# Optimization experiments

Hardware: AMD Instinct MI355X
Metric: run time of the kernel (lower is better)

Reference implementation:

```python
import jax, jax.numpy as jnp
import numpy as np


def _build_tree(N: int, n: int, seed: int = 0):
    """Random forest encoded as parent pointers + sibling ranks.

    parents:  int32 [N+1]; parents[i] in [0, i) for i>0, root(0) and sentinel(N) -> N.
    child_pos: int32 [N+1]; rank among siblings (in_edges order); >= n means the
               one-hot code is all zeros (matches torch.eye rows beyond n, and roots).
    """
    rng = np.random.default_rng(seed)
    parents = np.empty(N + 1, dtype=np.int32)
    parents[0] = N                      # root -> sentinel
    parents[1:N] = rng.integers(0, np.arange(1, N))  # parent of i is an earlier node
    parents[N] = N                      # sentinel self-loop

    pa = parents[:N].astype(np.int64)
    order = np.argsort(pa, kind="stable")
    sorted_pa = pa[order]
    _, first_idx, inv = np.unique(sorted_pa, return_index=True, return_inverse=True)
    rank = np.arange(N) - first_idx[inv]           # sibling rank within each parent group
    child_pos = np.empty(N + 1, dtype=np.int32)
    child_pos[order] = rank.astype(np.int32)
    child_pos[0] = n                    # root has no parent -> zero code
    child_pos[N] = n                    # sentinel -> zero code
    return parents, child_pos


def setup_inputs() -> dict:
    N, n, k = 262144, 32, 16
    parents, child_pos = _build_tree(N, n)
    return {
        "parents": jnp.asarray(parents),
        "child_pos": jnp.asarray(child_pos),
        "n": n,
        "k": k,
    }


def reference(parents, child_pos, n, k):
    """pos_embeds[node] = concat_{t=0..k-1} onehot(child_pos(ancestor_t(node)), n).

    This is the closed form of the original layer-by-layer scatter:
      pos[child, :n]  = eye row (sibling rank one-hot)
      pos[child, n:]  = pos[parent, :-n]
    Roots keep all-zero codes (child_pos = n -> out-of-range one-hot = zeros).
    """
    N = parents.shape[0] - 1

    def step(cur, _):
        code = jax.nn.one_hot(child_pos[cur], n, dtype=jnp.float32)  # [N, n]
        return parents[cur], code

    _, codes = jax.lax.scan(step, jnp.arange(N, dtype=parents.dtype), None, length=k)
    # codes: [k, N, n] -> [N, k*n] with slot 0 (own code) first
    return jnp.transpose(codes, (1, 0, 2)).reshape(N, k * n)
```

## Files before the change

kernel.cpp:

```cpp
#include <hip/hip_runtime.h>


#define NN 32
#define KK 16

typedef float f32x4 __attribute__((ext_vector_type(4)));

__global__ __launch_bounds__(256) void pe_fused_stride(
    const int* __restrict__ parents,
    const int* __restrict__ child_pos,
    f32x4* __restrict__ out4, int N, int n_waves)
{
    const int lane = (int)(threadIdx.x & 63);
    const int wid  = (int)((blockIdx.x * blockDim.x + threadIdx.x) >> 6);

    unsigned int c[4];
    {
        int cur = lane * n_waves + wid;
        if (cur >= N) cur = N;
        #pragma unroll
        for (int w = 0; w < 4; ++w) {
            unsigned int u = 0;
            #pragma unroll
            for (int b = 0; b < 4; ++b) {
                const int cp = child_pos[cur];
                const unsigned int byte = (cp < NN) ? (unsigned int)cp : 0xFFu;
                u |= byte << (8 * b);
                cur = parents[cur];
            }
            c[w] = u;
        }
    }

    const bool hi32 = (lane >= 32);
    const int  sh   = ((lane >> 3) & 3) * 8;
    const int  q4   = (lane & 7) * 4;

    f32x4* wout = out4 + (size_t)wid * 128 + lane;
    const size_t step = (size_t)n_waves * 128;

    #pragma unroll 4
    for (int j = 0; j < 64; ++j) {
        const unsigned s0 = (unsigned)__builtin_amdgcn_readlane((int)c[0], j);
        const unsigned s1 = (unsigned)__builtin_amdgcn_readlane((int)c[1], j);
        const unsigned s2 = (unsigned)__builtin_amdgcn_readlane((int)c[2], j);
        const unsigned s3 = (unsigned)__builtin_amdgcn_readlane((int)c[3], j);

        const int code0 = (int)(((hi32 ? s1 : s0) >> sh) & 0xFFu);
        const int code1 = (int)(((hi32 ? s3 : s2) >> sh) & 0xFFu);

        f32x4 v0, v1;
        v0.x = (code0 == q4    ) ? 1.0f : 0.0f;
        v0.y = (code0 == q4 + 1) ? 1.0f : 0.0f;
        v0.z = (code0 == q4 + 2) ? 1.0f : 0.0f;
        v0.w = (code0 == q4 + 3) ? 1.0f : 0.0f;
        v1.x = (code1 == q4    ) ? 1.0f : 0.0f;
        v1.y = (code1 == q4 + 1) ? 1.0f : 0.0f;
        v1.z = (code1 == q4 + 2) ? 1.0f : 0.0f;
        v1.w = (code1 == q4 + 3) ? 1.0f : 0.0f;

        wout[(size_t)j * step]      = v0;
        wout[(size_t)j * step + 64] = v1;
    }
}

extern "C" void kernel_launch(void* const* d_in, const int* in_sizes, int n_in,
                              void* d_out, int out_size, void* d_ws, size_t ws_size,
                              hipStream_t stream) {
    const int* parents   = (const int*)d_in[0];
    const int* child_pos = (const int*)d_in[1];
    f32x4* out4 = (f32x4*)d_out;

    const int N = in_sizes[0] - 1;
    const int n_waves = (N + 63) / 64;
    const int grid    = (n_waves + 3) / 4;

    pe_fused_stride<<<grid, 256, 0, stream>>>(parents, child_pos, out4, N, n_waves);
}
```

Baseline: 124.9 us.

## Pipeline ancestor-chain gathers with output stores across four node chunks per wave

```diff
diff --git a/kernel.cpp b/kernel.cpp
--- a/kernel.cpp
+++ b/kernel.cpp
@@ -6,17 +6,19 @@
 
 typedef float f32x4 __attribute__((ext_vector_type(4)));
 
-__global__ __launch_bounds__(256) void pe_fused_stride(
+__global__ __launch_bounds__(256) void pe_pipe(
     const int* __restrict__ parents,
     const int* __restrict__ child_pos,
-    f32x4* __restrict__ out4, int N, int n_waves)
+    f32x4* __restrict__ out4, int N)
 {
-    const int lane = (int)(threadIdx.x & 63);
-    const int wid  = (int)((blockIdx.x * blockDim.x + threadIdx.x) >> 6);
+    const int lane  = (int)(threadIdx.x & 63);
+    const int wid   = (int)((blockIdx.x * blockDim.x + threadIdx.x) >> 6);
+    const int wbase = wid * 256;
+    if (wbase >= N) return;
 
     unsigned int c[4];
     {
-        int cur = lane * n_waves + wid;
+        int cur = wbase + lane;
         if (cur >= N) cur = N;
         #pragma unroll
         for (int w = 0; w < 4; ++w) {
@@ -36,31 +38,67 @@
     const int  sh   = ((lane >> 3) & 3) * 8;
     const int  q4   = (lane & 7) * 4;
 
-    f32x4* wout = out4 + (size_t)wid * 128 + lane;
-    const size_t step = (size_t)n_waves * 128;
+    unsigned long long ulo = 0, uhi = 0;
+    int cp_p = 0, par_p = 0;
 
-    #pragma unroll 4
-    for (int j = 0; j < 64; ++j) {
-        const unsigned s0 = (unsigned)__builtin_amdgcn_readlane((int)c[0], j);
-        const unsigned s1 = (unsigned)__builtin_amdgcn_readlane((int)c[1], j);
-        const unsigned s2 = (unsigned)__builtin_amdgcn_readlane((int)c[2], j);
-        const unsigned s3 = (unsigned)__builtin_amdgcn_readlane((int)c[3], j);
+    #pragma unroll
+    for (int q = 0; q < 4; ++q) {
+        if (wbase + q * 64 >= N) break;
+        f32x4* wout = out4 + (size_t)(wbase + q * 64) * 128 + lane;
 
-        const int code0 = (int)(((hi32 ? s1 : s0) >> sh) & 0xFFu);
-        const int code1 = (int)(((hi32 ? s3 : s2) >> sh) & 0xFFu);
+        if (q < 3) {
+            int cur0 = wbase + (q + 1) * 64 + lane;
+            if (cur0 >= N) cur0 = N;
+            cp_p  = child_pos[cur0];
+            par_p = parents[cur0];
+            ulo = 0; uhi = 0;
+        }
 
-        f32x4 v0, v1;
-        v0.x = (code0 == q4    ) ? 1.0f : 0.0f;
-        v0.y = (code0 == q4 + 1) ? 1.0f : 0.0f;
-        v0.z = (code0 == q4 + 2) ? 1.0f : 0.0f;
-        v0.w = (code0 == q4 + 3) ? 1.0f : 0.0f;
-        v1.x = (code1 == q4    ) ? 1.0f : 0.0f;
-        v1.y = (code1 == q4 + 1) ? 1.0f : 0.0f;
-        v1.z = (code1 == q4 + 2) ? 1.0f : 0.0f;
-        v1.w = (code1 == q4 + 3) ? 1.0f : 0.0f;
+        #pragma unroll 1
+        for (int jj = 0; jj < 16; ++jj) {
+            if (q < 3 && jj > 0) {
+                const unsigned int byte = (cp_p < NN) ? (unsigned int)cp_p : 0xFFu;
+                const int r = jj - 1;
+                if (r < 8) ulo |= (unsigned long long)byte << (8 * r);
+                else       uhi |= (unsigned long long)byte << (8 * (r - 8));
+                const int cur = par_p;
+                cp_p  = child_pos[cur];
+                par_p = parents[cur];
+            }
+            #pragma unroll
+            for (int m = 0; m < 4; ++m) {
+                const int j = jj * 4 + m;
+                const unsigned s0 = (unsigned)__builtin_amdgcn_readlane((int)c[0], j);
+                const unsigned s1 = (unsigned)__builtin_amdgcn_readlane((int)c[1], j);
+                const unsigned s2 = (unsigned)__builtin_amdgcn_readlane((int)c[2], j);
+                const unsigned s3 = (unsigned)__builtin_amdgcn_readlane((int)c[3], j);
 
-        wout[(size_t)j * step]      = v0;
-        wout[(size_t)j * step + 64] = v1;
+                const int code0 = (int)(((hi32 ? s1 : s0) >> sh) & 0xFFu);
+                const int code1 = (int)(((hi32 ? s3 : s2) >> sh) & 0xFFu);
+
+                f32x4 v0, v1;
+                v0.x = (code0 == q4    ) ? 1.0f : 0.0f;
+                v0.y = (code0 == q4 + 1) ? 1.0f : 0.0f;
+                v0.z = (code0 == q4 + 2) ? 1.0f : 0.0f;
+                v0.w = (code0 == q4 + 3) ? 1.0f : 0.0f;
+                v1.x = (code1 == q4    ) ? 1.0f : 0.0f;
+                v1.y = (code1 == q4 + 1) ? 1.0f : 0.0f;
+                v1.z = (code1 == q4 + 2) ? 1.0f : 0.0f;
+                v1.w = (code1 == q4 + 3) ? 1.0f : 0.0f;
+
+                wout[(size_t)j * 128]      = v0;
+                wout[(size_t)j * 128 + 64] = v1;
+            }
+        }
+
+        if (q < 3) {
+            const unsigned int byte = (cp_p < NN) ? (unsigned int)cp_p : 0xFFu;
+            uhi |= (unsigned long long)byte << (8 * 7);
+            c[0] = (unsigned int)ulo;
+            c[1] = (unsigned int)(ulo >> 32);
+            c[2] = (unsigned int)uhi;
+            c[3] = (unsigned int)(uhi >> 32);
+        }
     }
 }
 
@@ -72,8 +110,8 @@
     f32x4* out4 = (f32x4*)d_out;
 
     const int N = in_sizes[0] - 1;
-    const int n_waves = (N + 63) / 64;
+    const int n_waves = (N + 255) / 256;
     const int grid    = (n_waves + 3) / 4;
 
-    pe_fused_stride<<<grid, 256, 0, stream>>>(parents, child_pos, out4, N, n_waves);
+    pe_pipe<<<grid, 256, 0, stream>>>(parents, child_pos, out4, N);
 }
```

Measured after the change: 112.5 us. -10.0%, faster.
